# Kernel optimization log

Measured on AMD Instinct MI355X. Metric: run time of the kernel, lower is better.

The kernel has to match this reference:

```python
import jax, jax.numpy as jnp
import numpy as np

B, L, H, NH = 2, 2048, 1024, 16
HD = H // NH  # head dim = 64


def setup_inputs() -> dict:
    key = jax.random.key(0)
    ks = jax.random.split(key, 8)
    s = 0.02  # small init scale for weights
    return {
        "q": jax.random.normal(ks[0], (B, L, H), jnp.float32),
        "k": jax.random.normal(ks[1], (B, L, H), jnp.float32),
        "v": jax.random.normal(ks[2], (B, L, H), jnp.float32),
        "attention_mask": jnp.zeros((B, NH, L, L), jnp.float32),
        "Wq": jax.random.normal(ks[3], (H, H), jnp.float32) * s,
        "bq": jnp.zeros((H,), jnp.float32),
        "Wk": jax.random.normal(ks[4], (H, H), jnp.float32) * s,
        "bk": jnp.zeros((H,), jnp.float32),
        "Wv": jax.random.normal(ks[5], (H, H), jnp.float32) * s,
        "bv": jnp.zeros((H,), jnp.float32),
        "Wo": jax.random.normal(ks[6], (H, H), jnp.float32) * s,
        "bo": jnp.zeros((H,), jnp.float32),
    }


def reference(q, k, v, attention_mask, Wq, bq, Wk, bk, Wv, bv, Wo, bo):
    # Conv1D (GPT-2 style) projections: x @ W + b
    query = q @ Wq + bq  # [B, L, H]
    key = k @ Wk + bk
    value = v @ Wv + bv
    # split heads -> [B, NH, L, HD]
    qh = query.reshape(B, L, NH, HD).transpose(0, 2, 1, 3)
    kh = key.reshape(B, L, NH, HD).transpose(0, 2, 1, 3)
    vh = value.reshape(B, L, NH, HD).transpose(0, 2, 1, 3)
    # scores: [B, NH, L, L]
    w = jnp.einsum("bhqd,bhkd->bhqk", qh, kh) / jnp.sqrt(jnp.float32(HD))
    w = w + attention_mask
    w = jax.nn.softmax(w, axis=-1)  # dropout p=0 -> identity
    out = jnp.einsum("bhqk,bhkd->bhqd", w, vh)  # [B, NH, L, HD]
    # merge heads -> [B, L, H]
    out = out.transpose(0, 2, 1, 3).reshape(B, L, H)
    return out @ Wo + bo
```

## Files before the change

### kernel.cpp

```cpp
#include <hip/hip_runtime.h>

#define NBATCH 2
#define LSEQ   2048
#define NH     16
#define HD     64
#define HDIM   1024
#define MTOK   4096

typedef unsigned short u16;
typedef __attribute__((ext_vector_type(8))) short bf16x8;
typedef __attribute__((ext_vector_type(4))) float f32x4;

__device__ __forceinline__ u16 f2bf(float f) {
  union { float f; unsigned int u; } x; x.f = f;
  return (u16)((x.u + 0x7fffu + ((x.u >> 16) & 1u)) >> 16);
}

__device__ __forceinline__ void gload_lds16(const void* g, void* l) {
  __builtin_amdgcn_global_load_lds(
      (const __attribute__((address_space(1))) unsigned int*)g,
      (__attribute__((address_space(3))) unsigned int*)l, 16, 0, 0);
}

__global__ void cvt_bf16_kernel(const float* __restrict__ in, u16* __restrict__ out) {
  int i = blockIdx.x * blockDim.x + threadIdx.x;
  float4 v = ((const float4*)in)[i];
  ushort4 o;
  o.x = f2bf(v.x); o.y = f2bf(v.y); o.z = f2bf(v.z); o.w = f2bf(v.w);
  ((ushort4*)out)[i] = o;
}

__global__ void wt_cvt_kernel(const float* __restrict__ W, u16* __restrict__ Wt) {
  __shared__ float tile[64][65];
  const int k0 = (blockIdx.x & 15) << 6;
  const int n0 = (blockIdx.x >> 4) << 6;
  const int t = threadIdx.x;
#pragma unroll
  for (int i = 0; i < 4; ++i) {
    int idx = t + i * 256;
    int r = idx >> 4, c = (idx & 15) << 2;
    float4 v = *(const float4*)&W[(size_t)(k0 + r) * HDIM + n0 + c];
    tile[r][c] = v.x; tile[r][c + 1] = v.y; tile[r][c + 2] = v.z; tile[r][c + 3] = v.w;
  }
  __syncthreads();
#pragma unroll
  for (int i = 0; i < 4; ++i) {
    int idx = t + i * 256;
    int r = idx >> 4, c = (idx & 15) << 2;
    ushort4 o;
    o.x = f2bf(tile[c][r]);     o.y = f2bf(tile[c + 1][r]);
    o.z = f2bf(tile[c + 2][r]); o.w = f2bf(tile[c + 3][r]);
    *(ushort4*)&Wt[(size_t)(n0 + r) * HDIM + k0 + c] = o;
  }
}

template <int MODE>
__device__ __forceinline__ void gemm_core(u16* As, u16* Bs,
    const u16* __restrict__ A, const u16* __restrict__ Bt,
    const float* __restrict__ bias, void* __restrict__ Cout) {
  const int tid = threadIdx.x;
  const int lane = tid & 63, wid = tid >> 6;
  const int l15 = lane & 15, g = lane >> 4;
  const int m0 = blockIdx.y * 128, n0 = blockIdx.x * 128;
  const int wr = wid >> 1, wc = wid & 1;
  f32x4 acc[4][4];
#pragma unroll
  for (int i = 0; i < 4; ++i)
#pragma unroll
    for (int j = 0; j < 4; ++j) acc[i][j] = (f32x4){0.f, 0.f, 0.f, 0.f};

  for (int t = 0; t < HDIM / 64; ++t) {
    const int k0 = t * 64;
    __syncthreads();
#pragma unroll
    for (int i = 0; i < 4; ++i) {
      const int row = wid * 32 + i * 8 + (lane >> 3);
      const int colb = (lane & 7) * 16;
      gload_lds16((const char*)(A + (size_t)(m0 + row) * HDIM + k0) + colb,
                  (char*)As + (wid * 32 + i * 8) * 128);
      gload_lds16((const char*)(Bt + (size_t)(n0 + row) * HDIM + k0) + colb,
                  (char*)Bs + (wid * 32 + i * 8) * 128);
    }
    __syncthreads();
#pragma unroll
    for (int ks = 0; ks < 2; ++ks) {
      bf16x8 a[4], b[4];
#pragma unroll
      for (int i = 0; i < 4; ++i) {
        const int row = wr * 64 + i * 16 + l15;
        a[i] = *(const bf16x8*)((const char*)As + row * 128 + ks * 64 + g * 16);
      }
#pragma unroll
      for (int j = 0; j < 4; ++j) {
        const int row = wc * 64 + j * 16 + l15;
        b[j] = *(const bf16x8*)((const char*)Bs + row * 128 + ks * 64 + g * 16);
      }
#pragma unroll
      for (int i = 0; i < 4; ++i)
#pragma unroll
        for (int j = 0; j < 4; ++j)
          acc[i][j] = __builtin_amdgcn_mfma_f32_16x16x32_bf16(a[i], b[j], acc[i][j], 0, 0, 0);
    }
  }
#pragma unroll
  for (int i = 0; i < 4; ++i) {
    const int mrow = m0 + wr * 64 + i * 16 + 4 * g;
#pragma unroll
    for (int j = 0; j < 4; ++j) {
      const int ncol = n0 + wc * 64 + j * 16 + l15;
      const float bb = bias[ncol];
      if (MODE == 3) {
        float* o = (float*)Cout;
#pragma unroll
        for (int r = 0; r < 4; ++r)
          o[(size_t)(mrow + r) * HDIM + ncol] = acc[i][j][r] + bb;
      } else if (MODE == 2) {
        const int bidx = mrow >> 11, l0 = mrow & (LSEQ - 1);
        const int h = ncol >> 6, d = ncol & 63;
        ushort4 o4;
        o4.x = f2bf(acc[i][j][0] + bb); o4.y = f2bf(acc[i][j][1] + bb);
        o4.z = f2bf(acc[i][j][2] + bb); o4.w = f2bf(acc[i][j][3] + bb);
        *(ushort4*)&((u16*)Cout)[(((size_t)bidx * NH + h) * HD + d) * LSEQ + l0] = o4;
      } else {
        const int h = ncol >> 6, d = ncol & 63;
        u16* o = (u16*)Cout;
#pragma unroll
        for (int r = 0; r < 4; ++r) {
          const int m = mrow + r;
          const int bidx = m >> 11, l = m & (LSEQ - 1);
          o[(((size_t)bidx * NH + h) * LSEQ + l) * HD + d] = f2bf(acc[i][j][r] + bb);
        }
      }
    }
  }
}

__global__ __launch_bounds__(256, 2) void proj_gemm_kernel(
    const u16* __restrict__ xq, const u16* __restrict__ xk, const u16* __restrict__ xv,
    const u16* __restrict__ WqT, const u16* __restrict__ WkT, const u16* __restrict__ WvT,
    const float* __restrict__ bq, const float* __restrict__ bk, const float* __restrict__ bv,
    u16* __restrict__ Qh, u16* __restrict__ Kh, u16* __restrict__ Vt) {
  __shared__ u16 As[128 * 64];
  __shared__ u16 Bs[128 * 64];
  if (blockIdx.z == 0)      gemm_core<0>(As, Bs, xq, WqT, bq, Qh);
  else if (blockIdx.z == 1) gemm_core<0>(As, Bs, xk, WkT, bk, Kh);
  else                      gemm_core<2>(As, Bs, xv, WvT, bv, Vt);
}

__global__ __launch_bounds__(256, 2) void out_gemm_kernel(
    const u16* __restrict__ A, const u16* __restrict__ WoT,
    const float* __restrict__ bo, float* __restrict__ out) {
  __shared__ u16 As[128 * 64];
  __shared__ u16 Bs[128 * 64];
  gemm_core<3>(As, Bs, A, WoT, bo, out);
}

__global__ __launch_bounds__(256, 4) void attn_kernel(
    const u16* __restrict__ Qh, const u16* __restrict__ Kh,
    const u16* __restrict__ Vt, const float* __restrict__ mask,
    u16* __restrict__ Out ) {
  __shared__ u16 Ks[64 * 64];
  __shared__ u16 Vs[64 * 64];
  __shared__ u16 Ps[4][16 * 64];
  const int lane = threadIdx.x & 63, w = threadIdx.x >> 6;
  const int l15 = lane & 15, g = lane >> 4;
  const int bh = blockIdx.y;
  const int q0 = blockIdx.x * 64 + w * 16;

  bf16x8 aq[2];
  {
    const u16* qbase = Qh + ((size_t)bh * LSEQ + q0 + l15) * HD;
    aq[0] = *(const bf16x8*)(qbase + g * 8);
    aq[1] = *(const bf16x8*)(qbase + 32 + g * 8);
  }
  f32x4 o_acc[4];
#pragma unroll
  for (int db = 0; db < 4; ++db) o_acc[db] = (f32x4){0.f, 0.f, 0.f, 0.f};
  float m_r[4], l_r[4];
#pragma unroll
  for (int r = 0; r < 4; ++r) { m_r[r] = -1e30f; l_r[r] = 0.f; }

  const size_t kbase = (size_t)bh * LSEQ * HD;
  const size_t vbase = (size_t)bh * HD * LSEQ;

  for (int t = 0; t < LSEQ / 64; ++t) {
    const int kv0 = t * 64;
    __syncthreads();
#pragma unroll
    for (int i = 0; i < 2; ++i) {
      const int row = w * 16 + i * 8 + (lane >> 3);
      const int colb = ((lane & 7) * 16) ^ ((row & 7) << 4);
      gload_lds16((const char*)(Kh + kbase + (size_t)(kv0 + row) * HD) + colb,
                  (char*)Ks + (w * 16 + i * 8) * 128);
      gload_lds16((const char*)(Vt + vbase + (size_t)row * LSEQ + kv0) + colb,
                  (char*)Vs + (w * 16 + i * 8) * 128);
    }
    __syncthreads();

    f32x4 s_acc[4];
#pragma unroll
    for (int nb = 0; nb < 4; ++nb) s_acc[nb] = (f32x4){0.f, 0.f, 0.f, 0.f};
#pragma unroll
    for (int ks = 0; ks < 2; ++ks) {
#pragma unroll
      for (int nb = 0; nb < 4; ++nb) {
        const int row = nb * 16 + l15;
        bf16x8 bk = *(const bf16x8*)((const char*)Ks + row * 128 +
                                     ((ks * 64 + g * 16) ^ ((row & 7) << 4)));
        s_acc[nb] = __builtin_amdgcn_mfma_f32_16x16x32_bf16(aq[ks], bk, s_acc[nb], 0, 0, 0);
      }
    }

    float pw[4][4];
#pragma unroll
    for (int r = 0; r < 4; ++r) {
      const int qg = q0 + 4 * g + r;
      const float* mrow = mask + ((size_t)bh * LSEQ + qg) * LSEQ + kv0;
      float v0 = s_acc[0][r] * 0.125f + mrow[l15];
      float v1 = s_acc[1][r] * 0.125f + mrow[16 + l15];
      float v2 = s_acc[2][r] * 0.125f + mrow[32 + l15];
      float v3 = s_acc[3][r] * 0.125f + mrow[48 + l15];
      float mm = fmaxf(fmaxf(v0, v1), fmaxf(v2, v3));
      mm = fmaxf(mm, __shfl_xor(mm, 1));
      mm = fmaxf(mm, __shfl_xor(mm, 2));
      mm = fmaxf(mm, __shfl_xor(mm, 4));
      mm = fmaxf(mm, __shfl_xor(mm, 8));
      const float mnew = fmaxf(m_r[r], mm);
      const float cf = __expf(m_r[r] - mnew);
      m_r[r] = mnew;
      float p0 = __expf(v0 - mnew), p1 = __expf(v1 - mnew);
      float p2 = __expf(v2 - mnew), p3 = __expf(v3 - mnew);
      pw[0][r] = p0; pw[1][r] = p1; pw[2][r] = p2; pw[3][r] = p3;
      float s0 = p0 + p1 + p2 + p3;
      s0 += __shfl_xor(s0, 1); s0 += __shfl_xor(s0, 2);
      s0 += __shfl_xor(s0, 4); s0 += __shfl_xor(s0, 8);
      l_r[r] = l_r[r] * cf + s0;
#pragma unroll
      for (int db = 0; db < 4; ++db) o_acc[db][r] *= cf;
    }

    u16* pbase = Ps[w];
#pragma unroll
    for (int r = 0; r < 4; ++r) {
      const int q = 4 * g + r;
#pragma unroll
      for (int nb = 0; nb < 4; ++nb) {
        const int colb = (nb * 32 + 2 * l15) ^ ((q & 7) << 4);
        *(u16*)((char*)pbase + q * 128 + colb) = f2bf(pw[nb][r]);
      }
    }
    __syncthreads();

#pragma unroll
    for (int s = 0; s < 2; ++s) {
      bf16x8 pa = *(const bf16x8*)((const char*)pbase + l15 * 128 +
                                   ((s * 64 + 16 * g) ^ ((l15 & 7) << 4)));
#pragma unroll
      for (int db = 0; db < 4; ++db) {
        const int row = db * 16 + l15;
        bf16x8 bv = *(const bf16x8*)((const char*)Vs + row * 128 +
                                     ((s * 64 + 16 * g) ^ ((row & 7) << 4)));
        o_acc[db] = __builtin_amdgcn_mfma_f32_16x16x32_bf16(pa, bv, o_acc[db], 0, 0, 0);
      }
    }
  }

  const int b = bh >> 4, h = bh & 15;
#pragma unroll
  for (int r = 0; r < 4; ++r) {
    const float inv = 1.f / l_r[r];
    const int qg = q0 + 4 * g + r;
    u16* orow = Out + ((size_t)(b * LSEQ + qg) * NH + h) * HD;
#pragma unroll
    for (int db = 0; db < 4; ++db)
      orow[db * 16 + l15] = f2bf(o_acc[db][r] * inv);
  }
}

extern "C" void kernel_launch(void* const* d_in, const int* in_sizes, int n_in,
                              void* d_out, int out_size, void* d_ws, size_t ws_size,
                              hipStream_t stream) {
  (void)in_sizes; (void)n_in; (void)out_size; (void)ws_size;
  const float* q    = (const float*)d_in[0];
  const float* k    = (const float*)d_in[1];
  const float* v    = (const float*)d_in[2];
  const float* mask = (const float*)d_in[3];
  const float* Wq   = (const float*)d_in[4];
  const float* bq   = (const float*)d_in[5];
  const float* Wk   = (const float*)d_in[6];
  const float* bk   = (const float*)d_in[7];
  const float* Wv   = (const float*)d_in[8];
  const float* bv   = (const float*)d_in[9];
  const float* Wo   = (const float*)d_in[10];
  const float* bo   = (const float*)d_in[11];
  float* out = (float*)d_out;

  char* ws = (char*)d_ws;
  const size_t XB = (size_t)MTOK * HDIM * 2;
  const size_t WB = (size_t)HDIM * HDIM * 2;
  u16* xq   = (u16*)(ws);
  u16* xk   = (u16*)(ws + XB);
  u16* xv   = (u16*)(ws + 2 * XB);
  u16* WqT  = (u16*)(ws + 3 * XB);
  u16* WkT  = (u16*)(ws + 3 * XB + WB);
  u16* WvT  = (u16*)(ws + 3 * XB + 2 * WB);
  u16* WoT  = (u16*)(ws + 3 * XB + 3 * WB);
  u16* Qh   = (u16*)(ws + 3 * XB + 4 * WB);
  u16* Kh   = (u16*)(ws + 4 * XB + 4 * WB);
  u16* Vt   = (u16*)(ws + 5 * XB + 4 * WB);
  u16* aout = (u16*)(ws + 6 * XB + 4 * WB);

  cvt_bf16_kernel<<<(MTOK * HDIM) / 4 / 256, 256, 0, stream>>>(q, xq);
  cvt_bf16_kernel<<<(MTOK * HDIM) / 4 / 256, 256, 0, stream>>>(k, xk);
  cvt_bf16_kernel<<<(MTOK * HDIM) / 4 / 256, 256, 0, stream>>>(v, xv);
  wt_cvt_kernel<<<256, 256, 0, stream>>>(Wq, WqT);
  wt_cvt_kernel<<<256, 256, 0, stream>>>(Wk, WkT);
  wt_cvt_kernel<<<256, 256, 0, stream>>>(Wv, WvT);
  wt_cvt_kernel<<<256, 256, 0, stream>>>(Wo, WoT);
  proj_gemm_kernel<<<dim3(HDIM / 128, MTOK / 128, 3), 256, 0, stream>>>(
      xq, xk, xv, WqT, WkT, WvT, bq, bk, bv, Qh, Kh, Vt);
  attn_kernel<<<dim3(LSEQ / 64, NBATCH * NH), 256, 0, stream>>>(Qh, Kh, Vt, mask, aout);
  out_gemm_kernel<<<dim3(HDIM / 128, MTOK / 128), 256, 0, stream>>>(aout, WoT, bo, out);
}
```

Measured before the change: 250.8 us.

## Double-buffer K/V tiles in attention, prefetch mask, batch conversion launches

The attention kernel now keeps two LDS buffers for K and V. It issues the global-to-LDS loads for the next tile before working on the current one, so each iteration needs one barrier instead of two. Mask values are loaded into registers at the top of each iteration to hide their latency, and the P tile writes are folded into the softmax loop, with an lgkmcnt wait replacing the barrier that came before the PV MMA. The three input conversions and four weight transposes are also merged into two launches using blockIdx.z. The cost is extra LDS per block, which may reduce occupancy, and the correctness of the async-load ordering now depends on the single remaining barrier.

```diff
diff --git a/kernel.cpp b/kernel.cpp
--- a/kernel.cpp
+++ b/kernel.cpp
@@ -22,15 +22,31 @@
       (__attribute__((address_space(3))) unsigned int*)l, 16, 0, 0);
 }
 
-__global__ void cvt_bf16_kernel(const float* __restrict__ in, u16* __restrict__ out) {
+__global__ void cvt3_kernel(const float* __restrict__ q, const float* __restrict__ k,
+                            const float* __restrict__ v, u16* __restrict__ xq,
+                            u16* __restrict__ xk, u16* __restrict__ xv) {
+  const float* in;
+  u16* out;
+  if (blockIdx.z == 0)      { in = q; out = xq; }
+  else if (blockIdx.z == 1) { in = k; out = xk; }
+  else                      { in = v; out = xv; }
   int i = blockIdx.x * blockDim.x + threadIdx.x;
-  float4 v = ((const float4*)in)[i];
+  float4 t = ((const float4*)in)[i];
   ushort4 o;
-  o.x = f2bf(v.x); o.y = f2bf(v.y); o.z = f2bf(v.z); o.w = f2bf(v.w);
+  o.x = f2bf(t.x); o.y = f2bf(t.y); o.z = f2bf(t.z); o.w = f2bf(t.w);
   ((ushort4*)out)[i] = o;
 }
 
-__global__ void wt_cvt_kernel(const float* __restrict__ W, u16* __restrict__ Wt) {
+__global__ void wt4_kernel(const float* __restrict__ W0, const float* __restrict__ W1,
+                           const float* __restrict__ W2, const float* __restrict__ W3,
+                           u16* __restrict__ T0, u16* __restrict__ T1,
+                           u16* __restrict__ T2, u16* __restrict__ T3) {
+  const float* W;
+  u16* Wt;
+  if (blockIdx.z == 0)      { W = W0; Wt = T0; }
+  else if (blockIdx.z == 1) { W = W1; Wt = T1; }
+  else if (blockIdx.z == 2) { W = W2; Wt = T2; }
+  else                      { W = W3; Wt = T3; }
   __shared__ float tile[64][65];
   const int k0 = (blockIdx.x & 15) << 6;
   const int n0 = (blockIdx.x >> 4) << 6;
@@ -159,8 +175,8 @@
     const u16* __restrict__ Qh, const u16* __restrict__ Kh,
     const u16* __restrict__ Vt, const float* __restrict__ mask,
     u16* __restrict__ Out ) {
-  __shared__ u16 Ks[64 * 64];
-  __shared__ u16 Vs[64 * 64];
+  __shared__ u16 Ks[2][64 * 64];
+  __shared__ u16 Vs[2][64 * 64];
   __shared__ u16 Ps[4][16 * 64];
   const int lane = threadIdx.x & 63, w = threadIdx.x >> 6;
   const int l15 = lane & 15, g = lane >> 4;
@@ -182,20 +198,39 @@
 
   const size_t kbase = (size_t)bh * LSEQ * HD;
   const size_t vbase = (size_t)bh * HD * LSEQ;
+  const int srow = w * 16 + (lane >> 3);
+  const int scolb = (lane & 7) * 16;
+
+#define STAGE(buf, tt) do {                                                    \
+    const int kv0_ = (tt) * 64;                                                \
+    _Pragma("unroll")                                                          \
+    for (int i_ = 0; i_ < 2; ++i_) {                                           \
+      const int row_ = srow + i_ * 8;                                          \
+      const int cb_ = scolb ^ ((row_ & 7) << 4);                               \
+      gload_lds16((const char*)(Kh + kbase + (size_t)(kv0_ + row_) * HD) + cb_,\
+                  (char*)Ks[buf] + (w * 16 + i_ * 8) * 128);                   \
+      gload_lds16((const char*)(Vt + vbase + (size_t)row_ * LSEQ + kv0_) + cb_,\
+                  (char*)Vs[buf] + (w * 16 + i_ * 8) * 128);                   \
+    }                                                                          \
+  } while (0)
+
+  STAGE(0, 0);
+  __syncthreads();
+
+  int cur = 0;
+  const float* mbase0 = mask + ((size_t)bh * LSEQ + q0 + 4 * g) * LSEQ + l15;
+  u16* pbase = Ps[w];
 
   for (int t = 0; t < LSEQ / 64; ++t) {
     const int kv0 = t * 64;
-    __syncthreads();
-#pragma unroll
-    for (int i = 0; i < 2; ++i) {
-      const int row = w * 16 + i * 8 + (lane >> 3);
-      const int colb = ((lane & 7) * 16) ^ ((row & 7) << 4);
-      gload_lds16((const char*)(Kh + kbase + (size_t)(kv0 + row) * HD) + colb,
-                  (char*)Ks + (w * 16 + i * 8) * 128);
-      gload_lds16((const char*)(Vt + vbase + (size_t)row * LSEQ + kv0) + colb,
-                  (char*)Vs + (w * 16 + i * 8) * 128);
-    }
-    __syncthreads();
+    if (t + 1 < LSEQ / 64) STAGE(cur ^ 1, t + 1);
+
+    float mv[4][4];
+#pragma unroll
+    for (int r = 0; r < 4; ++r)
+#pragma unroll
+      for (int nb = 0; nb < 4; ++nb)
+        mv[r][nb] = mbase0[(size_t)r * LSEQ + kv0 + nb * 16];
 
     f32x4 s_acc[4];
 #pragma unroll
@@ -205,21 +240,18 @@
 #pragma unroll
       for (int nb = 0; nb < 4; ++nb) {
         const int row = nb * 16 + l15;
-        bf16x8 bk = *(const bf16x8*)((const char*)Ks + row * 128 +
+        bf16x8 bk = *(const bf16x8*)((const char*)Ks[cur] + row * 128 +
                                      ((ks * 64 + g * 16) ^ ((row & 7) << 4)));
         s_acc[nb] = __builtin_amdgcn_mfma_f32_16x16x32_bf16(aq[ks], bk, s_acc[nb], 0, 0, 0);
       }
     }
 
-    float pw[4][4];
 #pragma unroll
     for (int r = 0; r < 4; ++r) {
-      const int qg = q0 + 4 * g + r;
-      const float* mrow = mask + ((size_t)bh * LSEQ + qg) * LSEQ + kv0;
-      float v0 = s_acc[0][r] * 0.125f + mrow[l15];
-      float v1 = s_acc[1][r] * 0.125f + mrow[16 + l15];
-      float v2 = s_acc[2][r] * 0.125f + mrow[32 + l15];
-      float v3 = s_acc[3][r] * 0.125f + mrow[48 + l15];
+      float v0 = s_acc[0][r] * 0.125f + mv[r][0];
+      float v1 = s_acc[1][r] * 0.125f + mv[r][1];
+      float v2 = s_acc[2][r] * 0.125f + mv[r][2];
+      float v3 = s_acc[3][r] * 0.125f + mv[r][3];
       float mm = fmaxf(fmaxf(v0, v1), fmaxf(v2, v3));
       mm = fmaxf(mm, __shfl_xor(mm, 1));
       mm = fmaxf(mm, __shfl_xor(mm, 2));
@@ -230,26 +262,21 @@
       m_r[r] = mnew;
       float p0 = __expf(v0 - mnew), p1 = __expf(v1 - mnew);
       float p2 = __expf(v2 - mnew), p3 = __expf(v3 - mnew);
-      pw[0][r] = p0; pw[1][r] = p1; pw[2][r] = p2; pw[3][r] = p3;
       float s0 = p0 + p1 + p2 + p3;
       s0 += __shfl_xor(s0, 1); s0 += __shfl_xor(s0, 2);
       s0 += __shfl_xor(s0, 4); s0 += __shfl_xor(s0, 8);
       l_r[r] = l_r[r] * cf + s0;
 #pragma unroll
       for (int db = 0; db < 4; ++db) o_acc[db][r] *= cf;
-    }
-
-    u16* pbase = Ps[w];
-#pragma unroll
-    for (int r = 0; r < 4; ++r) {
       const int q = 4 * g + r;
-#pragma unroll
-      for (int nb = 0; nb < 4; ++nb) {
-        const int colb = (nb * 32 + 2 * l15) ^ ((q & 7) << 4);
-        *(u16*)((char*)pbase + q * 128 + colb) = f2bf(pw[nb][r]);
-      }
-    }
-    __syncthreads();
+      const int qx = (q & 7) << 4;
+      *(u16*)((char*)pbase + q * 128 + ((0 + 2 * l15) ^ qx)) = f2bf(p0);
+      *(u16*)((char*)pbase + q * 128 + ((32 + 2 * l15) ^ qx)) = f2bf(p1);
+      *(u16*)((char*)pbase + q * 128 + ((64 + 2 * l15) ^ qx)) = f2bf(p2);
+      *(u16*)((char*)pbase + q * 128 + ((96 + 2 * l15) ^ qx)) = f2bf(p3);
+    }
+    asm volatile("s_waitcnt lgkmcnt(0)" ::: "memory");
+    __builtin_amdgcn_sched_barrier(0);
 
 #pragma unroll
     for (int s = 0; s < 2; ++s) {
@@ -258,12 +285,15 @@
 #pragma unroll
       for (int db = 0; db < 4; ++db) {
         const int row = db * 16 + l15;
-        bf16x8 bv = *(const bf16x8*)((const char*)Vs + row * 128 +
+        bf16x8 bv = *(const bf16x8*)((const char*)Vs[cur] + row * 128 +
                                      ((s * 64 + 16 * g) ^ ((row & 7) << 4)));
         o_acc[db] = __builtin_amdgcn_mfma_f32_16x16x32_bf16(pa, bv, o_acc[db], 0, 0, 0);
       }
     }
-  }
+    __syncthreads();
+    cur ^= 1;
+  }
+#undef STAGE
 
   const int b = bh >> 4, h = bh & 15;
 #pragma unroll
@@ -310,13 +340,10 @@
   u16* Vt   = (u16*)(ws + 5 * XB + 4 * WB);
   u16* aout = (u16*)(ws + 6 * XB + 4 * WB);
 
-  cvt_bf16_kernel<<<(MTOK * HDIM) / 4 / 256, 256, 0, stream>>>(q, xq);
-  cvt_bf16_kernel<<<(MTOK * HDIM) / 4 / 256, 256, 0, stream>>>(k, xk);
-  cvt_bf16_kernel<<<(MTOK * HDIM) / 4 / 256, 256, 0, stream>>>(v, xv);
-  wt_cvt_kernel<<<256, 256, 0, stream>>>(Wq, WqT);
-  wt_cvt_kernel<<<256, 256, 0, stream>>>(Wk, WkT);
-  wt_cvt_kernel<<<256, 256, 0, stream>>>(Wv, WvT);
-  wt_cvt_kernel<<<256, 256, 0, stream>>>(Wo, WoT);
+  cvt3_kernel<<<dim3((MTOK * HDIM) / 4 / 256, 1, 3), 256, 0, stream>>>(
+      q, k, v, xq, xk, xv);
+  wt4_kernel<<<dim3(256, 1, 4), 256, 0, stream>>>(
+      Wq, Wk, Wv, Wo, WqT, WkT, WvT, WoT);
   proj_gemm_kernel<<<dim3(HDIM / 128, MTOK / 128, 3), 256, 0, stream>>>(
       xq, xk, xv, WqT, WkT, WvT, bq, bk, bv, Qh, Kh, Vt);
   attn_kernel<<<dim3(LSEQ / 64, NBATCH * NH), 256, 0, stream>>>(Qh, Kh, Vt, mask, aout);
```

Result: no change. 246.2 us (-1.8%).
